# Kernel tuning notes

Measured on AMD Instinct MI355X. Metric: run time of the kernel, lower is better.

Reference implementation:

```python
import jax, jax.numpy as jnp
import numpy as np

N_NODES = 50000
N_EDGES = 800000
IN_DIM = 128
HID = 64
HEADS = 4
OUT_DIM = 128
NEG_SLOPE = 0.2


def setup_inputs() -> dict:
    key = jax.random.key(0)
    ks = jax.random.split(key, 11)
    x = jax.random.normal(ks[0], (N_NODES, IN_DIM), dtype=jnp.float32)
    edge_index = jax.random.randint(ks[1], (2, N_EDGES), 0, N_NODES, dtype=jnp.int64)
    s1 = 1.0 / np.sqrt(IN_DIM)
    s2 = 1.0 / np.sqrt(HEADS * HID)
    W1 = jax.random.normal(ks[2], (IN_DIM, HEADS * HID), dtype=jnp.float32) * s1
    a_src1 = jax.random.normal(ks[3], (HEADS, HID), dtype=jnp.float32) * s2
    a_dst1 = jax.random.normal(ks[4], (HEADS, HID), dtype=jnp.float32) * s2
    b1 = jnp.zeros((HEADS * HID,), dtype=jnp.float32)
    W2 = jax.random.normal(ks[5], (HEADS * HID, OUT_DIM), dtype=jnp.float32) * s2
    a_src2 = jax.random.normal(ks[6], (1, OUT_DIM), dtype=jnp.float32) * 0.1
    a_dst2 = jax.random.normal(ks[7], (1, OUT_DIM), dtype=jnp.float32) * 0.1
    b2 = jnp.zeros((OUT_DIM,), dtype=jnp.float32)
    return {"x": x, "edge_index": edge_index, "W1": W1, "a_src1": a_src1,
            "a_dst1": a_dst1, "b1": b1, "W2": W2, "a_src2": a_src2,
            "a_dst2": a_dst2, "b2": b2}


def _gat_conv(x, src, dst, W, a_src, a_dst, bias, heads, out_per_head, concat):
    n = x.shape[0]
    # linear projection per head: [N, H, F]
    h = (x @ W).reshape(n, heads, out_per_head)
    # per-node attention terms: [N, H]
    alpha_src = jnp.einsum('nhf,hf->nh', h, a_src)
    alpha_dst = jnp.einsum('nhf,hf->nh', h, a_dst)
    # edge logits with LeakyReLU: [E, H]
    e = jax.nn.leaky_relu(alpha_src[src] + alpha_dst[dst], NEG_SLOPE)
    # softmax over incoming edges of each destination node
    m = jax.ops.segment_max(e, dst, num_segments=n)  # [N, H]
    m = jnp.where(jnp.isfinite(m), m, 0.0)
    e = jnp.exp(e - m[dst])
    denom = jax.ops.segment_sum(e, dst, num_segments=n)  # [N, H]
    alpha = e / (denom[dst] + 1e-16)  # [E, H]
    # weighted scatter-aggregate of source messages
    out = jax.ops.segment_sum(h[src] * alpha[:, :, None], dst, num_segments=n)  # [N, H, F]
    if concat:
        out = out.reshape(n, heads * out_per_head)
    else:
        out = out.mean(axis=1)
    return out + bias


def reference(x, edge_index, W1, a_src1, a_dst1, b1, W2, a_src2, a_dst2, b2):
    n = x.shape[0]
    # PyG GATConv adds self-loops by default
    loops = jnp.arange(n, dtype=edge_index.dtype)
    src = jnp.concatenate([edge_index[0], loops])
    dst = jnp.concatenate([edge_index[1], loops])
    # dropout layers are identity in inference
    h = _gat_conv(x, src, dst, W1, a_src1, a_dst1, b1, HEADS, HID, True)
    h = jax.nn.elu(h)
    out = _gat_conv(h, src, dst, W2, a_src2, a_dst2, b2, 1, OUT_DIM, True)
    # F.normalize(p=2, dim=1)
    norm = jnp.linalg.norm(out, axis=1, keepdims=True)
    return out / jnp.maximum(norm, 1e-12)
```

## Files before the change

### kernel.cpp

```cpp
#include <hip/hip_runtime.h>
#include <hip/hip_fp16.h>
#include <math.h>

#define N_NODES 50000
#define N_EDGES 800000
#define ET (N_EDGES + N_NODES)
#define IN_DIM 128
#define HID 64
#define HEADS 4
#define C1 (HEADS * HID)
#define OUT_DIM 128
#define NEG_SLOPE 0.2f
#define MTILES 3125
#define SCAN_B 1024
#define NSCB 49

typedef _Float16 h8 __attribute__((ext_vector_type(8)));
typedef float f4 __attribute__((ext_vector_type(4)));

__device__ __forceinline__ float leaky(float v) { return fmaxf(v, NEG_SLOPE * v); }
__device__ __forceinline__ float elu(float v) { return v > 0.0f ? v : expm1f(v); }

__device__ __forceinline__ void fma_mix8(float* acc, h8 v, float w) {
    union { h8 h; int i[4]; } u; u.h = v;
#pragma unroll
    for (int k = 0; k < 4; ++k) {
        asm("v_fma_mix_f32 %0, %1, %2, %0 op_sel:[0,0,0] op_sel_hi:[1,0,0]"
            : "+v"(acc[2 * k]) : "v"(u.i[k]), "v"(w));
        asm("v_fma_mix_f32 %0, %1, %2, %0 op_sel:[1,0,0] op_sel_hi:[1,0,0]"
            : "+v"(acc[2 * k + 1]) : "v"(u.i[k]), "v"(w));
    }
}

__global__ void prep_kernel(const float* __restrict__ W1, const float* __restrict__ W2,
                            const int* __restrict__ dst, __half* __restrict__ w1t,
                            __half* __restrict__ w2t, int* __restrict__ cnt) {
    const int tid = blockIdx.x * blockDim.x + threadIdx.x;
    const int np = gridDim.x * blockDim.x;
    for (int i = tid; i < IN_DIM * C1; i += np) {
        int k1 = i >> 8, n1 = i & 255;
        w1t[n1 * IN_DIM + k1] = __float2half(W1[i]);
        int k2 = i >> 7, n2 = i & 127;
        w2t[n2 * C1 + k2] = __float2half(W2[i]);
    }
    for (int i = tid; i < ET; i += np) {
        int d = (i < N_EDGES) ? dst[i] : i - N_EDGES;
        atomicAdd(&cnt[d], 1);
    }
}

__global__ void scan_local(const int* __restrict__ cnt, int* __restrict__ lscan,
                           int* __restrict__ bsum) {
    __shared__ int wsum[16];
    const int t = threadIdx.x, lane = t & 63, wv = t >> 6;
    int idx = blockIdx.x * SCAN_B + t;
    int v = (idx < N_NODES) ? cnt[idx] : 0;
    int sc = v;
#pragma unroll
    for (int o = 1; o < 64; o <<= 1) {
        int u = __shfl_up(sc, o);
        if (lane >= o) sc += u;
    }
    if (lane == 63) wsum[wv] = sc;
    __syncthreads();
    if (t == 0) {
        int run = 0;
#pragma unroll
        for (int w = 0; w < 16; ++w) { int s = wsum[w]; wsum[w] = run; run += s; }
        bsum[blockIdx.x] = run;
    }
    __syncthreads();
    if (idx < N_NODES) lscan[idx] = sc + wsum[wv];
}

__global__ void scan_bsum(int* __restrict__ bsum) {
    const int t = threadIdx.x;
    int v = (t < NSCB) ? bsum[t] : 0;
    int sc = v;
#pragma unroll
    for (int o = 1; o < 64; o <<= 1) {
        int u = __shfl_up(sc, o);
        if (t >= o) sc += u;
    }
    if (t < NSCB) bsum[t] = sc - v;
}

__global__ void scan_final(const int* __restrict__ cnt, const int* __restrict__ lscan,
                           const int* __restrict__ bsum, int* __restrict__ rp,
                           int* __restrict__ cursor) {
    int idx = blockIdx.x * SCAN_B + threadIdx.x;
    if (idx == 0) rp[0] = 0;
    if (idx >= N_NODES) return;
    int inc = lscan[idx] + bsum[idx >> 10];
    rp[idx + 1] = inc;
    cursor[idx] = inc - cnt[idx];
}

__global__ void scatter_kernel(const int* __restrict__ src, const int* __restrict__ dst,
                               int* __restrict__ cursor, int* __restrict__ col_src) {
    int i = blockIdx.x * blockDim.x + threadIdx.x;
    if (i >= ET) return;
    int s, d;
    if (i < N_EDGES) { s = src[i]; d = dst[i]; } else { s = d = i - N_EDGES; }
    int pos = atomicAdd(&cursor[d], 1);
    col_src[pos] = s;
}

__global__ __launch_bounds__(256) void gemm1_mfma(
        const float* __restrict__ x, const __half* __restrict__ w1t,
        const float* __restrict__ aws, const float* __restrict__ awd,
        __half* __restrict__ hm, float* __restrict__ as1m, float* __restrict__ ad1m) {
    const int tile = blockIdx.x * 4 + (threadIdx.x >> 6);
    if (tile >= MTILES) return;
    const int lane = threadIdx.x & 63;
    const int m0 = tile * 16, lm = lane & 15, lq = lane >> 4;
    h8 afrag[4];
    const float4* xrow = (const float4*)(x + (size_t)(m0 + lm) * IN_DIM + lq * 8);
#pragma unroll
    for (int kt = 0; kt < 4; ++kt) {
        float4 a = xrow[kt * 8];
        float4 b = xrow[kt * 8 + 1];
        union { h8 v; __half2 p[4]; } u;
        u.p[0] = __floats2half2_rn(a.x, a.y);
        u.p[1] = __floats2half2_rn(a.z, a.w);
        u.p[2] = __floats2half2_rn(b.x, b.y);
        u.p[3] = __floats2half2_rn(b.z, b.w);
        afrag[kt] = u.v;
    }
    f4 acc[16];
#pragma unroll
    for (int nt = 0; nt < 16; ++nt) acc[nt] = (f4){0.f, 0.f, 0.f, 0.f};
#pragma unroll
    for (int nt = 0; nt < 16; ++nt) {
        const h8* brow = (const h8*)(w1t + (size_t)(nt * 16 + lm) * IN_DIM + lq * 8);
#pragma unroll
        for (int kt = 0; kt < 4; ++kt)
            acc[nt] = __builtin_amdgcn_mfma_f32_16x16x32_f16(afrag[kt], brow[kt * 4],
                                                             acc[nt], 0, 0, 0);
    }
    float sS[4][4] = {{0.f}}, sD[4][4] = {{0.f}};
#pragma unroll
    for (int nt = 0; nt < 16; ++nt) {
        int col = nt * 16 + lm;
        float wa = aws[col], wd = awd[col];
        int hd = nt >> 2;
        int f = col & 63;
#pragma unroll
        for (int r = 0; r < 4; ++r) {
            float v = acc[nt][r];
            hm[((size_t)hd * N_NODES + (m0 + lq * 4 + r)) * 64 + f] = __float2half(v);
            sS[hd][r] += v * wa;
            sD[hd][r] += v * wd;
        }
    }
#pragma unroll
    for (int o = 1; o < 16; o <<= 1) {
#pragma unroll
        for (int hd = 0; hd < 4; ++hd)
#pragma unroll
            for (int r = 0; r < 4; ++r) {
                sS[hd][r] += __shfl_xor(sS[hd][r], o);
                sD[hd][r] += __shfl_xor(sD[hd][r], o);
            }
    }
    if (lm == 0) {
#pragma unroll
        for (int r = 0; r < 4; ++r) {
            int row = m0 + lq * 4 + r;
#pragma unroll
            for (int hd = 0; hd < 4; ++hd) {
                as1m[hd * N_NODES + row] = sS[hd][r];
                ad1m[hd * N_NODES + row] = sD[hd][r];
            }
        }
    }
}

__global__ __launch_bounds__(256) void gemm2_mfma(
        const __half* __restrict__ ah, const __half* __restrict__ w2t,
        const float* __restrict__ aws, const float* __restrict__ awd,
        __half* __restrict__ h, float* __restrict__ as2, float* __restrict__ ad2) {
    const int tile = blockIdx.x * 4 + (threadIdx.x >> 6);
    if (tile >= MTILES) return;
    const int lane = threadIdx.x & 63;
    const int m0 = tile * 16, lm = lane & 15, lq = lane >> 4;
    h8 afrag[8];
    const h8* arow = (const h8*)(ah + (size_t)(m0 + lm) * C1 + lq * 8);
#pragma unroll
    for (int kt = 0; kt < 8; ++kt) afrag[kt] = arow[kt * 4];
    f4 acc[8];
#pragma unroll
    for (int nt = 0; nt < 8; ++nt) acc[nt] = (f4){0.f, 0.f, 0.f, 0.f};
#pragma unroll
    for (int nt = 0; nt < 8; ++nt) {
        const h8* brow = (const h8*)(w2t + (size_t)(nt * 16 + lm) * C1 + lq * 8);
#pragma unroll
        for (int kt = 0; kt < 8; ++kt)
            acc[nt] = __builtin_amdgcn_mfma_f32_16x16x32_f16(afrag[kt], brow[kt * 4],
                                                             acc[nt], 0, 0, 0);
    }
    float sS[4] = {0.f, 0.f, 0.f, 0.f}, sD[4] = {0.f, 0.f, 0.f, 0.f};
#pragma unroll
    for (int nt = 0; nt < 8; ++nt) {
        int col = nt * 16 + lm;
        float wa = aws[col], wd = awd[col];
#pragma unroll
        for (int r = 0; r < 4; ++r) {
            float v = acc[nt][r];
            h[(size_t)(m0 + lq * 4 + r) * OUT_DIM + col] = __float2half(v);
            sS[r] += v * wa;
            sD[r] += v * wd;
        }
    }
#pragma unroll
    for (int o = 1; o < 16; o <<= 1) {
#pragma unroll
        for (int r = 0; r < 4; ++r) {
            sS[r] += __shfl_xor(sS[r], o);
            sD[r] += __shfl_xor(sD[r], o);
        }
    }
    if (lm == 0) {
#pragma unroll
        for (int r = 0; r < 4; ++r) {
            int row = m0 + lq * 4 + r;
            as2[row] = sS[r];
            ad2[row] = sD[r];
        }
    }
}

__global__ __launch_bounds__(256) void aggregate1_fused(
        const int* __restrict__ rp, const int* __restrict__ cs,
        const __half* __restrict__ h1hm, const float* __restrict__ as1m,
        const float* __restrict__ ad1m, const float* __restrict__ b1,
        __half* __restrict__ out1h) {
    __shared__ int2 stg[8][32];
    const int head = blockIdx.x & 3, g = blockIdx.x >> 2;
    const int hw = threadIdx.x >> 5, li = threadIdx.x & 31;
    const int d = g * 8 + hw;
    const int e0 = rp[d], deg = rp[d + 1] - e0;
    const float* asb = as1m + head * N_NODES;
    const float adv = ad1m[head * N_NODES + d];
    const char* hb = (const char*)h1hm + (size_t)head * N_NODES * 128;
    const int es = li >> 3, fl = li & 7;
    const int lbyte = fl * 16;
    float acc[8] = {0.f, 0.f, 0.f, 0.f, 0.f, 0.f, 0.f, 0.f};
    float dsum = 0.f;
    for (int c0 = 0; c0 < deg; c0 += 32) {
        const int clen = min(32, deg - c0);
        int idx = c0 + li;
        bool valid = idx < deg;
        int s = valid ? cs[e0 + idx] : 0;
        float x = valid ? __expf(leaky(asb[s] + adv)) : 0.f;
        stg[hw][li] = make_int2(s << 7, __float_as_int(x));
        dsum += x;
        __builtin_amdgcn_wave_barrier();
        int j = 0;
        for (; j + 8 <= clen; j += 8) {
            int2 p0 = stg[hw][j + es];
            int2 p1 = stg[hw][j + 4 + es];
            h8 v0 = *(const h8*)(hb + p0.x + lbyte);
            h8 v1 = *(const h8*)(hb + p1.x + lbyte);
            fma_mix8(acc, v0, __int_as_float(p0.y));
            fma_mix8(acc, v1, __int_as_float(p1.y));
        }
        for (; j < clen; j += 4) {
            int2 p0 = stg[hw][j + es];
            h8 v0 = *(const h8*)(hb + p0.x + lbyte);
            fma_mix8(acc, v0, __int_as_float(p0.y));
        }
        __builtin_amdgcn_wave_barrier();
    }
#pragma unroll
    for (int f = 0; f < 8; ++f) {
        acc[f] += __shfl_xor(acc[f], 8);
        acc[f] += __shfl_xor(acc[f], 16);
    }
#pragma unroll
    for (int o = 16; o > 0; o >>= 1) dsum += __shfl_xor(dsum, o);
    if (es == 0) {
        float inv = 1.0f / (dsum + 1e-16f);
        float4 bA = ((const float4*)b1)[head * 16 + fl * 2];
        float4 bB = ((const float4*)b1)[head * 16 + fl * 2 + 1];
        h8 o;
        o[0] = (_Float16)elu(acc[0] * inv + bA.x);
        o[1] = (_Float16)elu(acc[1] * inv + bA.y);
        o[2] = (_Float16)elu(acc[2] * inv + bA.z);
        o[3] = (_Float16)elu(acc[3] * inv + bA.w);
        o[4] = (_Float16)elu(acc[4] * inv + bB.x);
        o[5] = (_Float16)elu(acc[5] * inv + bB.y);
        o[6] = (_Float16)elu(acc[6] * inv + bB.z);
        o[7] = (_Float16)elu(acc[7] * inv + bB.w);
        *(h8*)((char*)out1h + (size_t)d * 512 + head * 128 + lbyte) = o;
    }
}

__global__ __launch_bounds__(256) void aggregate2_fused(
        const int* __restrict__ rp, const int* __restrict__ cs,
        const __half* __restrict__ h2h, const float* __restrict__ as2,
        const float* __restrict__ ad2, const float* __restrict__ b2,
        float* __restrict__ out) {
    __shared__ int2 stg[8][32];
    const int hw = threadIdx.x >> 5, li = threadIdx.x & 31;
    const int d = blockIdx.x * 8 + hw;
    const int e0 = rp[d], deg = rp[d + 1] - e0;
    const float adv = ad2[d];
    const int q = li >> 4, lo = li & 15;
    const int lbyte = lo * 16;
    const char* hbase = (const char*)h2h;
    float acc[8] = {0.f, 0.f, 0.f, 0.f, 0.f, 0.f, 0.f, 0.f};
    float dsum = 0.f;
    for (int c0 = 0; c0 < deg; c0 += 32) {
        const int clen = min(32, deg - c0);
        int idx = c0 + li;
        bool valid = idx < deg;
        int s = valid ? cs[e0 + idx] : 0;
        float x = valid ? __expf(leaky(as2[s] + adv)) : 0.f;
        stg[hw][li] = make_int2(valid ? (s << 8) : 0, __float_as_int(x));
        dsum += x;
        __builtin_amdgcn_wave_barrier();
        int j = 0;
        for (; j + 4 <= clen; j += 4) {
            int2 p0 = stg[hw][j + q];
            int2 p1 = stg[hw][j + 2 + q];
            h8 v0 = *(const h8*)(hbase + p0.x + lbyte);
            h8 v1 = *(const h8*)(hbase + p1.x + lbyte);
            fma_mix8(acc, v0, __int_as_float(p0.y));
            fma_mix8(acc, v1, __int_as_float(p1.y));
        }
        for (; j < clen; j += 2) {
            int2 p0 = stg[hw][j + q];
            h8 v0 = *(const h8*)(hbase + p0.x + lbyte);
            fma_mix8(acc, v0, __int_as_float(p0.y));
        }
        __builtin_amdgcn_wave_barrier();
    }
#pragma unroll
    for (int f = 0; f < 8; ++f) acc[f] += __shfl_xor(acc[f], 16);
#pragma unroll
    for (int o = 16; o > 0; o >>= 1) dsum += __shfl_xor(dsum, o);
    if (q == 0) {
        float inv = 1.0f / (dsum + 1e-16f);
        float4 bA = ((const float4*)b2)[lo * 2];
        float4 bB = ((const float4*)b2)[lo * 2 + 1];
        float v0 = acc[0] * inv + bA.x, v1 = acc[1] * inv + bA.y;
        float v2 = acc[2] * inv + bA.z, v3 = acc[3] * inv + bA.w;
        float v4 = acc[4] * inv + bB.x, v5 = acc[5] * inv + bB.y;
        float v6 = acc[6] * inv + bB.z, v7 = acc[7] * inv + bB.w;
        float ss = v0 * v0 + v1 * v1 + v2 * v2 + v3 * v3 +
                   v4 * v4 + v5 * v5 + v6 * v6 + v7 * v7;
#pragma unroll
        for (int o = 1; o < 16; o <<= 1) ss += __shfl_xor(ss, o);
        float sc = 1.0f / fmaxf(sqrtf(ss), 1e-12f);
        float4* orow = (float4*)((char*)out + (size_t)d * 512 + lo * 32);
        orow[0] = make_float4(v0 * sc, v1 * sc, v2 * sc, v3 * sc);
        orow[1] = make_float4(v4 * sc, v5 * sc, v6 * sc, v7 * sc);
    }
}

extern "C" void kernel_launch(void* const* d_in, const int* in_sizes, int n_in,
                              void* d_out, int out_size, void* d_ws, size_t ws_size,
                              hipStream_t stream) {
    const float* x     = (const float*)d_in[0];
    const int*   edge  = (const int*)d_in[1];
    const int*   src   = edge;
    const int*   dst   = edge + N_EDGES;
    const float* W1    = (const float*)d_in[2];
    const float* aw_s1 = (const float*)d_in[3];
    const float* aw_d1 = (const float*)d_in[4];
    const float* b1    = (const float*)d_in[5];
    const float* W2    = (const float*)d_in[6];
    const float* aw_s2 = (const float*)d_in[7];
    const float* aw_d2 = (const float*)d_in[8];
    const float* b2    = (const float*)d_in[9];
    float* out = (float*)d_out;

    char* ws = (char*)d_ws;
    size_t off = 0;
    auto alloc = [&](size_t bytes) {
        void* p = ws + off;
        off += (bytes + 255) & ~(size_t)255;
        return p;
    };
    int*    col_src = (int*)alloc((size_t)ET * 4);
    int*    rp     = (int*)alloc((size_t)(N_NODES + 1) * 4);
    int*    cursor = (int*)alloc((size_t)N_NODES * 4);
    int*    cnt    = (int*)alloc((size_t)N_NODES * 4);
    int*    lscan  = (int*)alloc((size_t)NSCB * SCAN_B * 4);
    int*    bsum   = (int*)alloc((size_t)NSCB * 4);
    float*  as1    = (float*)alloc((size_t)N_NODES * HEADS * 4);
    float*  ad1    = (float*)alloc((size_t)N_NODES * HEADS * 4);
    float*  as2    = (float*)alloc((size_t)N_NODES * 4);
    float*  ad2    = (float*)alloc((size_t)N_NODES * 4);
    __half* w1t    = (__half*)alloc((size_t)IN_DIM * C1 * 2);
    __half* w2t    = (__half*)alloc((size_t)C1 * OUT_DIM * 2);
    __half* h1hm   = (__half*)alloc((size_t)N_NODES * C1 * 2);
    __half* out1h  = (__half*)alloc((size_t)N_NODES * C1 * 2);
    __half* h2h    = h1hm;
    (void)off;

    hipMemsetAsync(cnt, 0, (size_t)N_NODES * 4, stream);

    const int egrid = (ET + 255) / 256;

    prep_kernel<<<1024, 256, 0, stream>>>(W1, W2, dst, w1t, w2t, cnt);
    scan_local<<<NSCB, SCAN_B, 0, stream>>>(cnt, lscan, bsum);
    scan_bsum<<<1, 64, 0, stream>>>(bsum);
    scan_final<<<NSCB, SCAN_B, 0, stream>>>(cnt, lscan, bsum, rp, cursor);
    scatter_kernel<<<egrid, 256, 0, stream>>>(src, dst, cursor, col_src);

    gemm1_mfma<<<(MTILES + 3) / 4, 256, 0, stream>>>(x, w1t, aw_s1, aw_d1, h1hm, as1, ad1);
    aggregate1_fused<<<(N_NODES / 8) * HEADS, 256, 0, stream>>>(rp, col_src, h1hm, as1, ad1, b1, out1h);

    gemm2_mfma<<<(MTILES + 3) / 4, 256, 0, stream>>>(out1h, w2t, aw_s2, aw_d2, h2h, as2, ad2);
    aggregate2_fused<<<N_NODES / 8, 256, 0, stream>>>(rp, col_src, h2h, as2, ad2, b2, out);
}
```

Measured before the change: 356.4 us.

## Aggregate layer-1 over head pairs with pair-major features and interleaved attention scores

The layer-1 projection is now stored pair-major: two heads per 256-byte row instead of one head per 128-byte row, and the attention scores are stored as float2 per head pair. The first aggregation kernel now handles two heads per block, which halves the number of times CSR indices and edge weights are recomputed and gives each gathered row a longer contiguous read. The gather loops in both aggregation kernels are also unrolled to four loads in flight. The cost is more LDS per entry, a per-lane select between the two heads' weights, and higher register pressure.

```diff
diff --git a/kernel.cpp b/kernel.cpp
--- a/kernel.cpp
+++ b/kernel.cpp
@@ -109,7 +109,7 @@
 __global__ __launch_bounds__(256) void gemm1_mfma(
         const float* __restrict__ x, const __half* __restrict__ w1t,
         const float* __restrict__ aws, const float* __restrict__ awd,
-        __half* __restrict__ hm, float* __restrict__ as1m, float* __restrict__ ad1m) {
+        __half* __restrict__ hpm, float* __restrict__ as1m, float* __restrict__ ad1m) {
     const int tile = blockIdx.x * 4 + (threadIdx.x >> 6);
     if (tile >= MTILES) return;
     const int lane = threadIdx.x & 63;
@@ -144,11 +144,12 @@
         int col = nt * 16 + lm;
         float wa = aws[col], wd = awd[col];
         int hd = nt >> 2;
-        int f = col & 63;
+        int pr = nt >> 3;
+        int cip = col & 127;
 #pragma unroll
         for (int r = 0; r < 4; ++r) {
             float v = acc[nt][r];
-            hm[((size_t)hd * N_NODES + (m0 + lq * 4 + r)) * 64 + f] = __float2half(v);
+            hpm[((size_t)pr * N_NODES + (m0 + lq * 4 + r)) * 128 + cip] = __float2half(v);
             sS[hd][r] += v * wa;
             sD[hd][r] += v * wd;
         }
@@ -164,14 +165,15 @@
             }
     }
     if (lm == 0) {
+        float2* asp = (float2*)as1m;
+        float2* adp = (float2*)ad1m;
 #pragma unroll
         for (int r = 0; r < 4; ++r) {
             int row = m0 + lq * 4 + r;
-#pragma unroll
-            for (int hd = 0; hd < 4; ++hd) {
-                as1m[hd * N_NODES + row] = sS[hd][r];
-                ad1m[hd * N_NODES + row] = sD[hd][r];
-            }
+            asp[row]           = make_float2(sS[0][r], sS[1][r]);
+            asp[N_NODES + row] = make_float2(sS[2][r], sS[3][r]);
+            adp[row]           = make_float2(sD[0][r], sD[1][r]);
+            adp[N_NODES + row] = make_float2(sD[2][r], sD[3][r]);
         }
     }
 }
@@ -232,57 +234,67 @@
 
 __global__ __launch_bounds__(256) void aggregate1_fused(
         const int* __restrict__ rp, const int* __restrict__ cs,
-        const __half* __restrict__ h1hm, const float* __restrict__ as1m,
+        const __half* __restrict__ hpm, const float* __restrict__ as1m,
         const float* __restrict__ ad1m, const float* __restrict__ b1,
         __half* __restrict__ out1h) {
-    __shared__ int2 stg[8][32];
-    const int head = blockIdx.x & 3, g = blockIdx.x >> 2;
+    __shared__ int4 stg[8][32];
+    const int pair = blockIdx.x & 1, g = blockIdx.x >> 1;
     const int hw = threadIdx.x >> 5, li = threadIdx.x & 31;
     const int d = g * 8 + hw;
     const int e0 = rp[d], deg = rp[d + 1] - e0;
-    const float* asb = as1m + head * N_NODES;
-    const float adv = ad1m[head * N_NODES + d];
-    const char* hb = (const char*)h1hm + (size_t)head * N_NODES * 128;
-    const int es = li >> 3, fl = li & 7;
+    const float2* asb = (const float2*)as1m + (size_t)pair * N_NODES;
+    const float2 adv = ((const float2*)ad1m)[(size_t)pair * N_NODES + d];
+    const char* hb = (const char*)hpm + (size_t)pair * N_NODES * 256;
+    const int es = li >> 4, fl = li & 15;
+    const int hip = fl >> 3;
     const int lbyte = fl * 16;
     float acc[8] = {0.f, 0.f, 0.f, 0.f, 0.f, 0.f, 0.f, 0.f};
-    float dsum = 0.f;
+    float ds0 = 0.f, ds1 = 0.f;
     for (int c0 = 0; c0 < deg; c0 += 32) {
         const int clen = min(32, deg - c0);
         int idx = c0 + li;
         bool valid = idx < deg;
         int s = valid ? cs[e0 + idx] : 0;
-        float x = valid ? __expf(leaky(asb[s] + adv)) : 0.f;
-        stg[hw][li] = make_int2(s << 7, __float_as_int(x));
-        dsum += x;
+        float2 av = asb[s];
+        float x0 = valid ? __expf(leaky(av.x + adv.x)) : 0.f;
+        float x1 = valid ? __expf(leaky(av.y + adv.y)) : 0.f;
+        stg[hw][li] = make_int4(s << 8, __float_as_int(x0), __float_as_int(x1), 0);
+        ds0 += x0; ds1 += x1;
         __builtin_amdgcn_wave_barrier();
         int j = 0;
         for (; j + 8 <= clen; j += 8) {
-            int2 p0 = stg[hw][j + es];
-            int2 p1 = stg[hw][j + 4 + es];
+            int4 p0 = stg[hw][j + es];
+            int4 p1 = stg[hw][j + 2 + es];
+            int4 p2 = stg[hw][j + 4 + es];
+            int4 p3 = stg[hw][j + 6 + es];
             h8 v0 = *(const h8*)(hb + p0.x + lbyte);
             h8 v1 = *(const h8*)(hb + p1.x + lbyte);
-            fma_mix8(acc, v0, __int_as_float(p0.y));
-            fma_mix8(acc, v1, __int_as_float(p1.y));
-        }
-        for (; j < clen; j += 4) {
-            int2 p0 = stg[hw][j + es];
+            h8 v2 = *(const h8*)(hb + p2.x + lbyte);
+            h8 v3 = *(const h8*)(hb + p3.x + lbyte);
+            fma_mix8(acc, v0, __int_as_float(hip ? p0.z : p0.y));
+            fma_mix8(acc, v1, __int_as_float(hip ? p1.z : p1.y));
+            fma_mix8(acc, v2, __int_as_float(hip ? p2.z : p2.y));
+            fma_mix8(acc, v3, __int_as_float(hip ? p3.z : p3.y));
+        }
+        for (; j < clen; j += 2) {
+            int4 p0 = stg[hw][j + es];
             h8 v0 = *(const h8*)(hb + p0.x + lbyte);
-            fma_mix8(acc, v0, __int_as_float(p0.y));
+            fma_mix8(acc, v0, __int_as_float(hip ? p0.z : p0.y));
         }
         __builtin_amdgcn_wave_barrier();
     }
 #pragma unroll
-    for (int f = 0; f < 8; ++f) {
-        acc[f] += __shfl_xor(acc[f], 8);
-        acc[f] += __shfl_xor(acc[f], 16);
-    }
-#pragma unroll
-    for (int o = 16; o > 0; o >>= 1) dsum += __shfl_xor(dsum, o);
+    for (int f = 0; f < 8; ++f) acc[f] += __shfl_xor(acc[f], 16);
+#pragma unroll
+    for (int o = 16; o > 0; o >>= 1) {
+        ds0 += __shfl_xor(ds0, o);
+        ds1 += __shfl_xor(ds1, o);
+    }
     if (es == 0) {
-        float inv = 1.0f / (dsum + 1e-16f);
-        float4 bA = ((const float4*)b1)[head * 16 + fl * 2];
-        float4 bB = ((const float4*)b1)[head * 16 + fl * 2 + 1];
+        float den = hip ? ds1 : ds0;
+        float inv = 1.0f / (den + 1e-16f);
+        float4 bA = ((const float4*)b1)[pair * 32 + fl * 2];
+        float4 bB = ((const float4*)b1)[pair * 32 + fl * 2 + 1];
         h8 o;
         o[0] = (_Float16)elu(acc[0] * inv + bA.x);
         o[1] = (_Float16)elu(acc[1] * inv + bA.y);
@@ -292,7 +304,7 @@
         o[5] = (_Float16)elu(acc[5] * inv + bB.y);
         o[6] = (_Float16)elu(acc[6] * inv + bB.z);
         o[7] = (_Float16)elu(acc[7] * inv + bB.w);
-        *(h8*)((char*)out1h + (size_t)d * 512 + head * 128 + lbyte) = o;
+        *(h8*)((char*)out1h + (size_t)d * 512 + pair * 256 + lbyte) = o;
     }
 }
 
@@ -321,13 +333,19 @@
         dsum += x;
         __builtin_amdgcn_wave_barrier();
         int j = 0;
-        for (; j + 4 <= clen; j += 4) {
+        for (; j + 8 <= clen; j += 8) {
             int2 p0 = stg[hw][j + q];
             int2 p1 = stg[hw][j + 2 + q];
+            int2 p2 = stg[hw][j + 4 + q];
+            int2 p3 = stg[hw][j + 6 + q];
             h8 v0 = *(const h8*)(hbase + p0.x + lbyte);
             h8 v1 = *(const h8*)(hbase + p1.x + lbyte);
+            h8 v2 = *(const h8*)(hbase + p2.x + lbyte);
+            h8 v3 = *(const h8*)(hbase + p3.x + lbyte);
             fma_mix8(acc, v0, __int_as_float(p0.y));
             fma_mix8(acc, v1, __int_as_float(p1.y));
+            fma_mix8(acc, v2, __int_as_float(p2.y));
+            fma_mix8(acc, v3, __int_as_float(p3.y));
         }
         for (; j < clen; j += 2) {
             int2 p0 = stg[hw][j + q];
@@ -395,9 +413,9 @@
     float*  ad2    = (float*)alloc((size_t)N_NODES * 4);
     __half* w1t    = (__half*)alloc((size_t)IN_DIM * C1 * 2);
     __half* w2t    = (__half*)alloc((size_t)C1 * OUT_DIM * 2);
-    __half* h1hm   = (__half*)alloc((size_t)N_NODES * C1 * 2);
+    __half* hpm    = (__half*)alloc((size_t)N_NODES * C1 * 2);
     __half* out1h  = (__half*)alloc((size_t)N_NODES * C1 * 2);
-    __half* h2h    = h1hm;
+    __half* h2h    = hpm;
     (void)off;
 
     hipMemsetAsync(cnt, 0, (size_t)N_NODES * 4, stream);
@@ -410,8 +428,8 @@
     scan_final<<<NSCB, SCAN_B, 0, stream>>>(cnt, lscan, bsum, rp, cursor);
     scatter_kernel<<<egrid, 256, 0, stream>>>(src, dst, cursor, col_src);
 
-    gemm1_mfma<<<(MTILES + 3) / 4, 256, 0, stream>>>(x, w1t, aw_s1, aw_d1, h1hm, as1, ad1);
-    aggregate1_fused<<<(N_NODES / 8) * HEADS, 256, 0, stream>>>(rp, col_src, h1hm, as1, ad1, b1, out1h);
+    gemm1_mfma<<<(MTILES + 3) / 4, 256, 0, stream>>>(x, w1t, aw_s1, aw_d1, hpm, as1, ad1);
+    aggregate1_fused<<<(N_NODES / 8) * 2, 256, 0, stream>>>(rp, col_src, hpm, as1, ad1, b1, out1h);
 
     gemm2_mfma<<<(MTILES + 3) / 4, 256, 0, stream>>>(out1h, w2t, aw_s2, aw_d2, h2h, as2, ad2);
     aggregate2_fused<<<N_NODES / 8, 256, 0, stream>>>(rp, col_src, h2h, as2, ad2, b2, out);
```

After: 349.0 us. 2.1% less time.
